# Optimization experiments

Hardware: AMD Instinct MI355X
Metric: run time of the kernel (lower is better)

The kernel has to match this reference:

```python
import jax, jax.numpy as jnp
import numpy as np

N = 40000          # nodes per type (dev, repo)
H, D = 8, 64       # heads, head dim
HID = H * D        # 512 hidden channels
OUT = 256
N_CONVS = 4        # 2 towers (res, link) x 2 layers
EDGE_TYPES = [(0, 1), (1, 0), (0, 0)]  # (src_type, dst_type)
SQRT_D = float(np.sqrt(D))


def _lin(x, w, b):
    return x @ w + b


def _seg_softmax(a, idx, n):
    m = jax.ops.segment_max(a, idx, num_segments=n)
    e = jnp.exp(a - m[idx])
    s = jax.ops.segment_sum(e, idx, num_segments=n)
    return e / (s[idx] + 1e-16)


def _hgt_conv(xs, edges, kw, kb, qw, qb, vw, vb, aw, ab, skip, a_rel, m_rel, p_rel):
    # xs: [x_dev, x_repo] each [N, HID]; edges: list of [2, E]
    k = [_lin(xs[t], kw[t], kb[t]).reshape(-1, H, D) for t in range(2)]
    q = [_lin(xs[t], qw[t], qb[t]).reshape(-1, H, D) for t in range(2)]
    v = [_lin(xs[t], vw[t], vb[t]).reshape(-1, H, D) for t in range(2)]
    out = [jnp.zeros_like(k[0]), jnp.zeros_like(k[1])]
    for r, (st, dt) in enumerate(EDGE_TYPES):
        src, dst = edges[r][0], edges[r][1]
        k_rel = jnp.einsum('nhd,hde->nhe', k[st], a_rel[r])
        v_rel = jnp.einsum('nhd,hde->nhe', v[st], m_rel[r])
        alpha = (q[dt][dst] * k_rel[src]).sum(-1) * p_rel[r] / SQRT_D  # [E, H]
        alpha = _seg_softmax(alpha, dst, N)
        msg = v_rel[src] * alpha[..., None]                            # [E, H, D]
        out[dt] = out[dt] + jax.ops.segment_sum(msg, dst, num_segments=N)
    res = []
    for t in range(2):
        o = _lin(jax.nn.gelu(out[t].reshape(-1, HID), approximate=False), aw[t], ab[t])
        g = jax.nn.sigmoid(skip[t])
        res.append(g * o + (1.0 - g) * xs[t])
    return res


def setup_inputs() -> dict:
    key = jax.random.key(0)
    ks = iter(jax.random.split(key, 48))
    def nrm(shape, scale=1.0):
        return jax.random.normal(next(ks), shape, dtype=jnp.float32) * scale
    E1, E2, E3, EP = 250000, 250000, 150000, 100000
    inp = {}
    inp['x_dev'] = nrm((N, HID))
    inp['x_repo'] = nrm((N, HID))
    inp['ei_dr'] = jax.random.randint(next(ks), (2, E1), 0, N, dtype=jnp.int32)
    inp['ei_rd'] = jax.random.randint(next(ks), (2, E2), 0, N, dtype=jnp.int32)
    inp['ei_dd'] = jax.random.randint(next(ks), (2, E3), 0, N, dtype=jnp.int32)
    inp['pos_edge'] = jax.random.randint(next(ks), (2, EP), 0, N, dtype=jnp.int32)
    inp['neg_edge'] = jax.random.randint(next(ks), (2, EP), 0, N, dtype=jnp.int32)
    s = 1.0 / np.sqrt(HID)
    for nm in ('k', 'q', 'v', 'a'):
        inp[nm + '_w'] = nrm((N_CONVS, 2, HID, HID), s)
        inp[nm + '_b'] = jnp.zeros((N_CONVS, 2, HID), jnp.float32)
    inp['skip'] = jnp.ones((N_CONVS, 2), jnp.float32)
    sd = 1.0 / np.sqrt(D)
    inp['a_rel'] = nrm((N_CONVS, 3, H, D, D), sd)
    inp['m_rel'] = nrm((N_CONVS, 3, H, D, D), sd)
    inp['p_rel'] = jnp.ones((N_CONVS, 3, H), jnp.float32)
    inp['reg_w1'] = nrm((HID, OUT), s); inp['reg_b1'] = jnp.zeros((OUT,), jnp.float32)
    inp['reg_w2'] = nrm((OUT, 1), 1.0 / np.sqrt(OUT)); inp['reg_b2'] = jnp.zeros((1,), jnp.float32)
    inp['src_w'] = nrm((HID, OUT), s); inp['src_b'] = jnp.zeros((OUT,), jnp.float32)
    inp['dst_w'] = nrm((HID, OUT), s); inp['dst_b'] = jnp.zeros((OUT,), jnp.float32)
    inp['fin_w'] = nrm((OUT, 1), 1.0 / np.sqrt(OUT)); inp['fin_b'] = jnp.zeros((1,), jnp.float32)
    return inp


def reference(x_dev, x_repo, ei_dr, ei_rd, ei_dd, pos_edge, neg_edge,
              k_w, k_b, q_w, q_b, v_w, v_b, a_w, a_b, skip,
              a_rel, m_rel, p_rel,
              reg_w1, reg_b1, reg_w2, reg_b2,
              src_w, src_b, dst_w, dst_b, fin_w, fin_b):
    edges = [ei_dr, ei_rd, ei_dd]

    def embed(conv_ids):
        xs = [x_dev, x_repo]
        for c in conv_ids:
            xs = _hgt_conv(xs, edges, k_w[c], k_b[c], q_w[c], q_b[c], v_w[c], v_b[c],
                           a_w[c], a_b[c], skip[c], a_rel[c], m_rel[c], p_rel[c])
            xs = [jax.nn.leaky_relu(x, 0.01) for x in xs]
        return xs

    res = embed([0, 1])   # embedding_res tower
    lnk = embed([2, 3])   # embedding_link tower
    emb_dev = res[0] + lnk[0]
    emb_repo = res[1] + lnk[1]

    fit_dev = _lin(_lin(emb_dev, reg_w1, reg_b1), reg_w2, reg_b2).squeeze(-1)
    fit_repo = _lin(_lin(emb_repo, reg_w1, reg_b1), reg_w2, reg_b2).squeeze(-1)

    def link(zs, zd):
        h = _lin(zs, src_w, src_b) * _lin(zd, dst_w, dst_b)
        return jax.nn.sigmoid(_lin(h, fin_w, fin_b)).squeeze(-1)

    pos = link(emb_dev[pos_edge[0]], emb_repo[pos_edge[1]])
    neg = link(emb_dev[neg_edge[0]], emb_repo[neg_edge[1]])
    score = jnp.concatenate([pos, neg], axis=0)
    return (fit_dev, fit_repo, score)
```

## Files before the change

kernel.cpp:

```cpp
#include <hip/hip_runtime.h>
#include <math.h>

#define NNODES 40000
#define NB ((size_t)20480000)
#define RPS 40004

typedef __attribute__((ext_vector_type(8))) short bf16x8;
typedef __attribute__((ext_vector_type(4))) float f32x4;

__device__ __forceinline__ ushort f2bf(float f) {
  unsigned u = __float_as_uint(f);
  u += 0x7FFFu + ((u >> 16) & 1u);
  return (ushort)(u >> 16);
}
__device__ __forceinline__ float b2f(ushort h) {
  return __uint_as_float((unsigned)h << 16);
}
__device__ __forceinline__ float gelu_f(float x) {
  return 0.5f * x * (1.0f + erff(x * 0.70710678118654752440f));
}

__device__ __forceinline__ void gll16(const ushort* g, ushort* l) {
  __builtin_amdgcn_global_load_lds(
      (const __attribute__((address_space(1))) unsigned int*)(const void*)g,
      (__attribute__((address_space(3))) unsigned int*)(void*)l, 16, 0, 0);
}

template<int EPI>
__global__ __launch_bounds__(256)
void gemm_bf16_kernel(const ushort* __restrict__ Av, const ushort* __restrict__ Bt,
                      const float* __restrict__ bias,
                      ushort* __restrict__ C0, ushort* __restrict__ C1,
                      int M, int PW, int RS,
                      const ushort* __restrict__ xprev, const float* __restrict__ skipv,
                      int nwgx)
{
  const int K = 512;
  __shared__ char smem[32768];
  ushort* Sm = (ushort*)smem;
  float*  Es = (float*)smem;

  const int nwg = (int)gridDim.x;
  const int q8 = nwg >> 3, r8 = nwg & 7;
  const int xcd = (int)blockIdx.x & 7, i8 = (int)blockIdx.x >> 3;
  const int logical = (xcd < r8 ? xcd * (q8 + 1) : r8 * (q8 + 1) + (xcd - r8) * q8) + i8;
  const int bm = (logical / nwgx) * 128;
  const int bnl = (logical % nwgx) * 128;
  const int pan = (bnl >= PW) ? 1 : 0;
  const int bn = bnl - pan * PW;
  ushort* __restrict__ C = pan ? C1 : C0;

  const int tid = threadIdx.x, lane = tid & 63, wave = tid >> 6;
  const int wr = (wave >> 1) * 64, wc = (wave & 1) * 64;
  const int fr = lane & 15, fq = lane >> 4;
  f32x4 acc[4][4] = {};

  const int rdsw = (fq ^ ((fr >> 1) & 3)) * 8;
  const int csrc = ((lane & 3) ^ ((lane >> 3) & 3)) * 8;
  const int r0 = wave * 32 + (lane >> 2);
  int ra0 = bm + r0;      if (ra0 >= M) ra0 = M - 1;
  int ra1 = bm + r0 + 16; if (ra1 >= M) ra1 = M - 1;
  const ushort* ga0 = Av + (size_t)ra0 * K + csrc;
  const ushort* ga1 = Av + (size_t)ra1 * K + csrc;
  const ushort* gb0 = Bt + (size_t)(bnl + r0) * K + csrc;
  const ushort* gb1 = Bt + (size_t)(bnl + r0 + 16) * K + csrc;
  ushort* la0[2] = {Sm + wave * 1024,        Sm + 8192 + wave * 1024};
  ushort* la1[2] = {la0[0] + 512,            la0[1] + 512};
  ushort* lb0[2] = {Sm + 4096 + wave * 1024, Sm + 12288 + wave * 1024};
  ushort* lb1[2] = {lb0[0] + 512,            lb0[1] + 512};

  gll16(ga0, la0[0]); gll16(ga1, la1[0]); gll16(gb0, lb0[0]); gll16(gb1, lb1[0]);
  ga0 += 32; ga1 += 32; gb0 += 32; gb1 += 32;
  gll16(ga0, la0[1]); gll16(ga1, la1[1]); gll16(gb0, lb0[1]); gll16(gb1, lb1[1]);
  ga0 += 32; ga1 += 32; gb0 += 32; gb1 += 32;

  #pragma unroll
  for (int it = 0; it < 16; ++it) {
    const int cur = it & 1;
    if (it < 15) asm volatile("s_waitcnt vmcnt(4)" ::: "memory");
    else         asm volatile("s_waitcnt vmcnt(0)" ::: "memory");
    __builtin_amdgcn_s_barrier();
    const ushort* Ab = Sm + cur * 8192;
    const ushort* Bb = Ab + 4096;
    bf16x8 af[4], bfv[4];
    #pragma unroll
    for (int i = 0; i < 4; ++i) {
      af[i]  = *(const bf16x8*)&Ab[(wr + i * 16 + fr) * 32 + rdsw];
      bfv[i] = *(const bf16x8*)&Bb[(wc + i * 16 + fr) * 32 + rdsw];
    }
    asm volatile("s_waitcnt lgkmcnt(0)" ::: "memory");
    __builtin_amdgcn_s_barrier();
    if (it < 14) {
      gll16(ga0, la0[cur]); gll16(ga1, la1[cur]); gll16(gb0, lb0[cur]); gll16(gb1, lb1[cur]);
      ga0 += 32; ga1 += 32; gb0 += 32; gb1 += 32;
    }
    #pragma unroll
    for (int mi = 0; mi < 4; ++mi)
      #pragma unroll
      for (int ni = 0; ni < 4; ++ni)
        acc[mi][ni] = __builtin_amdgcn_mfma_f32_16x16x32_bf16(af[mi], bfv[ni], acc[mi][ni], 0, 0, 0);
  }
  __syncthreads();

  float gate = 0.f, og = 0.f;
  if (EPI == 2) { gate = 1.f / (1.f + __expf(-skipv[0])); og = 1.f - gate; }
  #pragma unroll
  for (int qr = 0; qr < 4; ++qr) {
    __syncthreads();
    #pragma unroll
    for (int mi = 0; mi < 4; ++mi) {
      if (((wr + mi * 16) >> 5) != qr) continue;
      const int lr = ((wr + mi * 16) & 31) + fq * 4;
      #pragma unroll
      for (int ni = 0; ni < 4; ++ni) {
        const int col = wc + ni * 16 + fr;
        #pragma unroll
        for (int r = 0; r < 4; ++r)
          Es[(lr + r) * 132 + col] = acc[mi][ni][r];
      }
    }
    __syncthreads();
    const int lrow = tid >> 3;
    const int c0 = (tid & 7) * 16;
    const int grow = bm + qr * 32 + lrow;
    if (grow < M) {
      float v[16];
      #pragma unroll
      for (int j = 0; j < 4; ++j)
        *(float4*)&v[j * 4] = *(const float4*)&Es[lrow * 132 + c0 + j * 4];
      if (EPI == 1 || EPI == 2) {
        #pragma unroll
        for (int j = 0; j < 4; ++j) {
          float4 b4 = *(const float4*)(bias + bnl + c0 + j * 4);
          v[j*4] += b4.x; v[j*4+1] += b4.y; v[j*4+2] += b4.z; v[j*4+3] += b4.w;
        }
      }
      size_t base = (size_t)grow * RS + bn + c0;
      if (EPI == 2) {
        uint4 x0 = *(const uint4*)(xprev + base);
        uint4 x1 = *(const uint4*)(xprev + base + 8);
        #pragma unroll
        for (int j = 0; j < 8; ++j) {
          unsigned w = (j < 4) ? ((const unsigned*)&x0)[j] : ((const unsigned*)&x1)[j - 4];
          float a  = gate * v[2*j]   + og * __uint_as_float(w << 16);
          float bq = gate * v[2*j+1] + og * __uint_as_float(w & 0xFFFF0000u);
          v[2*j]   = a  > 0.f ? a  : 0.01f * a;
          v[2*j+1] = bq > 0.f ? bq : 0.01f * bq;
        }
      }
      if (EPI == 4) {
        uint4 x0 = *(const uint4*)(C + base);
        uint4 x1 = *(const uint4*)(C + base + 8);
        #pragma unroll
        for (int j = 0; j < 8; ++j) {
          unsigned w = (j < 4) ? ((const unsigned*)&x0)[j] : ((const unsigned*)&x1)[j - 4];
          v[2*j]   += __uint_as_float(w << 16);
          v[2*j+1] += __uint_as_float(w & 0xFFFF0000u);
        }
      }
      ushort ob[16];
      #pragma unroll
      for (int j = 0; j < 16; ++j) ob[j] = f2bf(v[j]);
      *(uint4*)(C + base)     = *(uint4*)&ob[0];
      *(uint4*)(C + base + 8) = *(uint4*)&ob[8];
    }
  }
}

__global__ __launch_bounds__(256)
void transpose_w_batch(const float* __restrict__ q_w, const float* __restrict__ a_w,
                       const float* __restrict__ src_w, const float* __restrict__ dst_w,
                       ushort* __restrict__ wqT, ushort* __restrict__ waT,
                       ushort* __restrict__ srcwT, ushort* __restrict__ dstwT)
{
  const int z = blockIdx.z;
  const float* W; ushort* Wt; int N;
  if (z < 8)       { W = q_w + (size_t)z * 262144;       Wt = wqT + (size_t)z * 262144;       N = 512; }
  else if (z < 16) { W = a_w + (size_t)(z - 8) * 262144; Wt = waT + (size_t)(z - 8) * 262144; N = 512; }
  else if (z == 16){ W = src_w; Wt = srcwT; N = 256; }
  else             { W = dst_w; Wt = dstwT; N = 256; }
  int bn = blockIdx.x * 32, bk = blockIdx.y * 32;
  if (bn >= N) return;
  __shared__ float t[32][33];
  int x = threadIdx.x & 31, y = threadIdx.x >> 5;
  #pragma unroll
  for (int yy = y; yy < 32; yy += 8) t[yy][x] = W[(size_t)(bk + yy) * N + bn + x];
  __syncthreads();
  #pragma unroll
  for (int yy = y; yy < 32; yy += 8) Wt[(size_t)(bn + yy) * 512 + bk + x] = f2bf(t[x][yy]);
}

__global__ __launch_bounds__(256)
void fold_rel_batch(const float* __restrict__ k_w, const float* __restrict__ k_b,
                    const float* __restrict__ v_w, const float* __restrict__ v_b,
                    const float* __restrict__ a_rel, const float* __restrict__ m_rel,
                    ushort* __restrict__ wkvT, float* __restrict__ bfuse)
{
  const int z = blockIdx.z;
  const int kv = z / 12, i = z % 12;
  const int c = i / 3, r = i % 3;
  const int st_tab[3] = {0, 1, 0};
  const int stp = st_tab[r];
  const float* Win  = (kv ? v_w : k_w) + (size_t)(c * 2 + stp) * 262144;
  const float* bin  = (kv ? v_b : k_b) + (size_t)(c * 2 + stp) * 512;
  const float* Arel = (kv ? m_rel : a_rel) + (size_t)i * 32768;
  const int h = blockIdx.x, kc = blockIdx.y;
  ushort* W2t = wkvT + (size_t)i * 524288 + (size_t)(h >> 2) * 262144
              + (size_t)(kv * 256 + (h & 3) * 64) * 512;
  float*  b2  = bfuse + i * 1024 + (h >> 2) * 512 + kv * 256 + (h & 3) * 64;

  __shared__ float Wl[64][65];
  __shared__ float Al[4096];
  for (int j = threadIdx.x; j < 4096; j += 256) Al[j] = Arel[(size_t)h * 4096 + j];
  {
    const int kk = threadIdx.x >> 2, d0 = (threadIdx.x & 3) * 16;
    const float* src = Win + (size_t)(kc * 64 + kk) * 512 + h * 64 + d0;
    #pragma unroll
    for (int j = 0; j < 4; ++j)
      *(float4*)&Wl[kk][d0 + j * 4] = *(const float4*)(src + j * 4);
  }
  __syncthreads();
  const int wave = threadIdx.x >> 6, lane = threadIdx.x & 63;
  #pragma unroll 4
  for (int rr = 0; rr < 16; ++rr) {
    const int e = wave * 16 + rr;
    float acc = 0.f;
    #pragma unroll
    for (int d = 0; d < 64; ++d) acc = fmaf(Wl[lane][d], Al[d * 64 + e], acc);
    W2t[(size_t)e * 512 + kc * 64 + lane] = f2bf(acc);
  }
  if (kc == 0 && wave == 0) {
    float acc = 0.f;
    #pragma unroll
    for (int d = 0; d < 64; ++d) acc = fmaf(bin[h * 64 + d], Al[d * 64 + lane], acc);
    b2[lane] = acc;
  }
}

__global__ __launch_bounds__(256)
void make_wfit_kernel(const float* __restrict__ w1, const float* __restrict__ b1,
                      const float* __restrict__ w2, const float* __restrict__ b2,
                      float* __restrict__ wfit)
{
  for (int k = threadIdx.x; k < 512; k += 256) {
    float acc = 0.f;
    for (int j = 0; j < 256; ++j) acc = fmaf(w1[(size_t)k * 256 + j], w2[j], acc);
    wfit[k] = acc;
  }
  if (threadIdx.x == 0) {
    float acc = 0.f;
    for (int j = 0; j < 256; ++j) acc = fmaf(b1[j], w2[j], acc);
    wfit[512] = acc + b2[0];
  }
}

__global__ __launch_bounds__(256)
void hist_batch(const int* __restrict__ d0, const int* __restrict__ d1,
                const int* __restrict__ d2, unsigned* __restrict__ cnt3)
{
  const int z = blockIdx.z;
  const int* dst = (z == 0) ? d0 : (z == 1) ? d1 : d2;
  const int E = (z == 2) ? 150000 : 250000;
  unsigned* cnt = cnt3 + (size_t)z * NNODES;
  for (int i = blockIdx.x * 256 + threadIdx.x; i < E; i += gridDim.x * 256)
    atomicAdd(&cnt[dst[i]], 1u);
}

__global__ __launch_bounds__(256)
void scan_batch(const unsigned* __restrict__ cnt3, unsigned* __restrict__ rowptr3,
                unsigned* __restrict__ woff3)
{
  const int z = blockIdx.x;
  const unsigned* cnt = cnt3 + (size_t)z * NNODES;
  unsigned* rowptr = rowptr3 + (size_t)z * RPS;
  unsigned* woff   = woff3 + (size_t)z * NNODES;
  __shared__ unsigned csum[256];
  const int t = threadIdx.x;
  const int lo = t * 160, hi = (lo + 160 < NNODES) ? lo + 160 : NNODES;
  unsigned s = 0;
  for (int i = lo; i < hi; i += 4) {
    uint4 v = *(const uint4*)&cnt[i];
    s += v.x + v.y + v.z + v.w;
  }
  csum[t] = s;
  __syncthreads();
  if (t == 0) {
    unsigned run = 0;
    for (int j = 0; j < 256; ++j) { unsigned v = csum[j]; csum[j] = run; run += v; }
    rowptr[NNODES] = run;
  }
  __syncthreads();
  unsigned run = csum[t];
  for (int i = lo; i < hi; i += 4) {
    uint4 cv = *(const uint4*)&cnt[i];
    uint4 rp;
    rp.x = run; run += cv.x;
    rp.y = run; run += cv.y;
    rp.z = run; run += cv.z;
    rp.w = run; run += cv.w;
    *(uint4*)&rowptr[i] = rp;
    *(uint4*)&woff[i]   = rp;
  }
}

__global__ __launch_bounds__(256)
void fill_batch(const int* __restrict__ e0, const int* __restrict__ e1,
                const int* __restrict__ e2, unsigned* __restrict__ woff3,
                ushort* __restrict__ srcord)
{
  const int z = blockIdx.z;
  const int* e = (z == 0) ? e0 : (z == 1) ? e1 : e2;
  const int E = (z == 2) ? 150000 : 250000;
  const int* src = e;
  const int* dst = e + E;
  unsigned* woff = woff3 + (size_t)z * NNODES;
  ushort* ord = srcord + ((z == 0) ? 0 : (z == 1) ? 250000 : 500000);
  for (int i = blockIdx.x * 256 + threadIdx.x; i < E; i += gridDim.x * 256) {
    unsigned slot = atomicAdd(&woff[dst[i]], 1u);
    ord[slot] = (ushort)src[i];
  }
}

template<int ACCUM, int GELU>
__global__ __launch_bounds__(256)
void fused_edge_kernel(const ushort* __restrict__ q, const ushort* __restrict__ KVh,
                      const unsigned* __restrict__ rowptr, const ushort* __restrict__ srcord,
                      const float* __restrict__ prel, int hs,
                      const ushort* __restrict__ accin, ushort* __restrict__ outp)
{
  int d = (int)((blockIdx.x * 256u + threadIdx.x) >> 6);
  int lane = threadIdx.x & 63;
  if (d >= NNODES) return;
  unsigned start = rowptr[d], end = rowptr[d + 1];
  const int hl = lane >> 4;
  const int off = hl * 64 + (lane & 15) * 4;
  const float pscale = prel[hs * 4 + hl] * 0.125f;
  const size_t obase = (size_t)d * 512 + hs * 256 + off;

  uint2 qv = *(const uint2*)(q + obase);
  float qf0 = __uint_as_float(qv.x << 16),         qf1 = __uint_as_float(qv.x & 0xFFFF0000u);
  float qf2 = __uint_as_float(qv.y << 16),         qf3 = __uint_as_float(qv.y & 0xFFFF0000u);

  float m = -3e38f, ssum = 0.f;
  float a0 = 0.f, a1 = 0.f, a2 = 0.f, a3 = 0.f;
  if (start < end) {
    int sn = (int)srcord[start];
    const ushort* r0 = KVh + (size_t)sn * 512 + off;
    uint2 kv_c = *(const uint2*)r0;
    uint2 vv_c = *(const uint2*)(r0 + 256);
    const unsigned last = end - 1;
    for (unsigned idx = start; idx < end; ++idx) {
      unsigned idxn = (idx < last) ? idx + 1 : last;
      int sn2 = (int)srcord[idxn];
      const ushort* rn = KVh + (size_t)sn2 * 512 + off;
      uint2 kv_n = *(const uint2*)rn;
      uint2 vv_n = *(const uint2*)(rn + 256);
      float dot =      qf0 * __uint_as_float(kv_c.x << 16);
      dot = fmaf(qf1, __uint_as_float(kv_c.x & 0xFFFF0000u), dot);
      dot = fmaf(qf2, __uint_as_float(kv_c.y << 16),         dot);
      dot = fmaf(qf3, __uint_as_float(kv_c.y & 0xFFFF0000u), dot);
      dot += __shfl_xor(dot, 1);
      dot += __shfl_xor(dot, 2);
      dot += __shfl_xor(dot, 4);
      dot += __shfl_xor(dot, 8);
      float a = dot * pscale;
      if (a > m) {
        float r = __expf(m - a);
        ssum *= r; a0 *= r; a1 *= r; a2 *= r; a3 *= r;
        m = a;
      }
      float w = __expf(a - m);
      ssum += w;
      a0 = fmaf(w, __uint_as_float(vv_c.x << 16),         a0);
      a1 = fmaf(w, __uint_as_float(vv_c.x & 0xFFFF0000u), a1);
      a2 = fmaf(w, __uint_as_float(vv_c.y << 16),         a2);
      a3 = fmaf(w, __uint_as_float(vv_c.y & 0xFFFF0000u), a3);
      kv_c = kv_n; vv_c = vv_n;
    }
  }
  float rs = 1.f / (ssum + 1e-16f);
  float o0 = a0 * rs, o1 = a1 * rs, o2 = a2 * rs, o3 = a3 * rs;
  if (ACCUM) {
    uint2 old = *(const uint2*)(accin + obase);
    o0 += __uint_as_float(old.x << 16);  o1 += __uint_as_float(old.x & 0xFFFF0000u);
    o2 += __uint_as_float(old.y << 16);  o3 += __uint_as_float(old.y & 0xFFFF0000u);
  }
  if (GELU) { o0 = gelu_f(o0); o1 = gelu_f(o1); o2 = gelu_f(o2); o3 = gelu_f(o3); }
  uint2 ov;
  ov.x = (unsigned)f2bf(o0) | ((unsigned)f2bf(o1) << 16);
  ov.y = (unsigned)f2bf(o2) | ((unsigned)f2bf(o3) << 16);
  *(uint2*)(outp + obase) = ov;
}

template<int ACCUM, int GELU>
__global__ __launch_bounds__(256)
void fused_edge_full_kernel(const ushort* __restrict__ q, const ushort* __restrict__ KVf,
                            const unsigned* __restrict__ rowptr, const ushort* __restrict__ srcord,
                            const float* __restrict__ prel,
                            const ushort* __restrict__ accin, ushort* __restrict__ outp)
{
  int d = (int)((blockIdx.x * 256u + threadIdx.x) >> 6);
  int lane = threadIdx.x & 63;
  if (d >= NNODES) return;
  unsigned start = rowptr[d], end = rowptr[d + 1];
  const int h = lane >> 3, sub = lane & 7;
  const int koff = (h >> 2) * 512 + (h & 3) * 64 + sub * 8;
  const float pscale = prel[h] * 0.125f;
  const size_t obase = (size_t)d * 512 + h * 64 + sub * 8;

  uint4 qv = *(const uint4*)(q + obase);
  const unsigned* pq = (const unsigned*)&qv;
  float qf[8];
  #pragma unroll
  for (int j = 0; j < 4; ++j) {
    qf[2*j]   = __uint_as_float(pq[j] << 16);
    qf[2*j+1] = __uint_as_float(pq[j] & 0xFFFF0000u);
  }

  float m = -3e38f, ssum = 0.f;
  float av[8] = {};
  if (start < end) {
    int sn = (int)srcord[start];
    const ushort* r0 = KVf + (size_t)sn * 1024 + koff;
    uint4 kv_c = *(const uint4*)r0;
    uint4 vv_c = *(const uint4*)(r0 + 256);
    const unsigned last = end - 1;
    for (unsigned idx = start; idx < end; ++idx) {
      unsigned idxn = (idx < last) ? idx + 1 : last;
      int sn2 = (int)srcord[idxn];
      const ushort* rn = KVf + (size_t)sn2 * 1024 + koff;
      uint4 kv_n = *(const uint4*)rn;
      uint4 vv_n = *(const uint4*)(rn + 256);
      const unsigned* pk = (const unsigned*)&kv_c;
      float dot = 0.f;
      #pragma unroll
      for (int j = 0; j < 4; ++j) {
        dot = fmaf(qf[2*j],   __uint_as_float(pk[j] << 16),         dot);
        dot = fmaf(qf[2*j+1], __uint_as_float(pk[j] & 0xFFFF0000u), dot);
      }
      dot += __shfl_xor(dot, 1);
      dot += __shfl_xor(dot, 2);
      dot += __shfl_xor(dot, 4);
      float a = dot * pscale;
      if (a > m) {
        float r = __expf(m - a);
        ssum *= r;
        #pragma unroll
        for (int j = 0; j < 8; ++j) av[j] *= r;
        m = a;
      }
      float w = __expf(a - m);
      ssum += w;
      const unsigned* pv = (const unsigned*)&vv_c;
      #pragma unroll
      for (int j = 0; j < 4; ++j) {
        av[2*j]   = fmaf(w, __uint_as_float(pv[j] << 16),         av[2*j]);
        av[2*j+1] = fmaf(w, __uint_as_float(pv[j] & 0xFFFF0000u), av[2*j+1]);
      }
      kv_c = kv_n; vv_c = vv_n;
    }
  }
  float rs = 1.f / (ssum + 1e-16f);
  float o[8];
  #pragma unroll
  for (int j = 0; j < 8; ++j) o[j] = av[j] * rs;
  if (ACCUM) {
    uint4 old = *(const uint4*)(accin + obase);
    const unsigned* po = (const unsigned*)&old;
    #pragma unroll
    for (int j = 0; j < 4; ++j) {
      o[2*j]   += __uint_as_float(po[j] << 16);
      o[2*j+1] += __uint_as_float(po[j] & 0xFFFF0000u);
    }
  }
  if (GELU) {
    #pragma unroll
    for (int j = 0; j < 8; ++j) o[j] = gelu_f(o[j]);
  }
  ushort ob[8];
  #pragma unroll
  for (int j = 0; j < 8; ++j) ob[j] = f2bf(o[j]);
  *(uint4*)(outp + obase) = *(uint4*)ob;
}

template<int MODE>
__global__ __launch_bounds__(256)
void fitdot_kernel(const ushort* __restrict__ cur, const float* __restrict__ wfit,
                   float* __restrict__ out, int M)
{
  int row = (int)((blockIdx.x * 256u + threadIdx.x) >> 6);
  int lane = threadIdx.x & 63;
  if (row >= M) return;
  uint4 v = *(const uint4*)(cur + (size_t)row * 512 + lane * 8);
  const unsigned* pv = (const unsigned*)&v;
  float wreg[8];
  *(float4*)wreg       = *(const float4*)(wfit + lane * 8);
  *(float4*)(wreg + 4) = *(const float4*)(wfit + lane * 8 + 4);
  float acc = 0.f;
  #pragma unroll
  for (int j = 0; j < 4; ++j) {
    acc = fmaf(__uint_as_float(pv[j] << 16),         wreg[2 * j],     acc);
    acc = fmaf(__uint_as_float(pv[j] & 0xFFFF0000u), wreg[2 * j + 1], acc);
  }
  #pragma unroll
  for (int off = 1; off < 64; off <<= 1) acc += __shfl_xor(acc, off);
  if (lane == 0) {
    if (MODE == 0) out[row] = acc;
    else           out[row] += acc + wfit[512];
  }
}

__global__ __launch_bounds__(256)
void link_score_kernel(const ushort* __restrict__ se, const ushort* __restrict__ de,
                       const float* __restrict__ sb, const float* __restrict__ db,
                       const int* __restrict__ si, const int* __restrict__ di,
                       int E, const float* __restrict__ fw, const float* __restrict__ fb,
                       float* __restrict__ out)
{
  int wv = (int)((blockIdx.x * 256u + threadIdx.x) >> 6);
  int lane = threadIdx.x & 63;
  if (wv >= E) return;
  int s = si[wv], d = di[wv];
  ushort4 a = *(const ushort4*)(se + (size_t)s * 256 + lane * 4);
  ushort4 b = *(const ushort4*)(de + (size_t)d * 256 + lane * 4);
  float4 s4 = *(const float4*)(sb + lane * 4);
  float4 d4 = *(const float4*)(db + lane * 4);
  float4 w4 = *(const float4*)(fw + lane * 4);
  float acc = (b2f(a.x) + s4.x) * (b2f(b.x) + d4.x) * w4.x
            + (b2f(a.y) + s4.y) * (b2f(b.y) + d4.y) * w4.y
            + (b2f(a.z) + s4.z) * (b2f(b.z) + d4.z) * w4.z
            + (b2f(a.w) + s4.w) * (b2f(b.w) + d4.w) * w4.w;
  #pragma unroll
  for (int off = 1; off < 64; off <<= 1) acc += __shfl_xor(acc, off);
  if (lane == 0) out[wv] = 1.f / (1.f + __expf(-(acc + fb[0])));
}

__global__ __launch_bounds__(256)
void f32_to_bf16_kernel(const float* __restrict__ in, ushort* __restrict__ out, int n4)
{
  for (int i = blockIdx.x * 256 + threadIdx.x; i < n4; i += gridDim.x * 256) {
    float4 v = ((const float4*)in)[i];
    ushort4 o; o.x = f2bf(v.x); o.y = f2bf(v.y); o.z = f2bf(v.z); o.w = f2bf(v.w);
    ((ushort4*)out)[i] = o;
  }
}

__global__ void diag_kernel(float* __restrict__ out, float v)
{
  if (threadIdx.x == 0 && blockIdx.x == 0) out[0] = v;
}

extern "C" void kernel_launch(void* const* d_in, const int* in_sizes, int n_in,
                              void* d_out, int out_size, void* d_ws, size_t ws_size,
                              hipStream_t stream)
{
  const float* x_dev  = (const float*)d_in[0];
  const float* x_repo = (const float*)d_in[1];
  const int* ei[3] = {(const int*)d_in[2], (const int*)d_in[3], (const int*)d_in[4]};
  const int  Ecnt[3] = {250000, 250000, 150000};
  const int* pos_e = (const int*)d_in[5];
  const int* neg_e = (const int*)d_in[6];
  const float* k_w = (const float*)d_in[7];  const float* k_b = (const float*)d_in[8];
  const float* q_w = (const float*)d_in[9];  const float* q_b = (const float*)d_in[10];
  const float* v_w = (const float*)d_in[11]; const float* v_b = (const float*)d_in[12];
  const float* a_w = (const float*)d_in[13]; const float* a_b = (const float*)d_in[14];
  const float* skip  = (const float*)d_in[15];
  const float* a_rel = (const float*)d_in[16];
  const float* m_rel = (const float*)d_in[17];
  const float* p_rel = (const float*)d_in[18];
  const float* reg_w1 = (const float*)d_in[19]; const float* reg_b1 = (const float*)d_in[20];
  const float* reg_w2 = (const float*)d_in[21]; const float* reg_b2 = (const float*)d_in[22];
  const float* src_w  = (const float*)d_in[23]; const float* src_b  = (const float*)d_in[24];
  const float* dst_w  = (const float*)d_in[25]; const float* dst_b  = (const float*)d_in[26];
  const float* fin_w  = (const float*)d_in[27]; const float* fin_b  = (const float*)d_in[28];
  float* out = (float*)d_out;

  const size_t SE = (size_t)NNODES * 256;
  const size_t tail_bytes =
      (size_t)8 * 262144 * 2
    + (size_t)8 * 262144 * 2
    + (size_t)12 * 524288 * 2
    + 131072ull * 2 * 2
    + 12288ull * 4 + 516ull * 4
    + (size_t)3 * RPS * 4
    + 650000ull * 2 + 4
    + (size_t)3 * NNODES * 4 * 2;
  const size_t need_full = (6 * NB + 2 * SE) * 2 + tail_bytes;
  const size_t need_half = (5 * NB + 2 * SE) * 2 + tail_bytes;
  int FULL;
  if      (ws_size >= need_full) FULL = 1;
  else if (ws_size >= need_half) FULL = 0;
  else {
    diag_kernel<<<1, 64, 0, stream>>>(out, 1000.0f + (float)(ws_size / 1000000));
    return;
  }

  ushort* st   = (ushort*)d_ws;
  ushort* cur0 = st;
  ushort* cur1 = st + NB;
  ushort* S1   = st + 2 * NB;
  ushort* S2   = st + 3 * NB;
  ushort* KV   = st + 4 * NB;
  ushort* se   = st + (FULL ? 6 : 5) * NB;
  ushort* de   = se + SE;
  ushort* wqT   = de + SE;
  ushort* waT   = wqT + (size_t)8 * 262144;
  ushort* wkvT  = waT + (size_t)8 * 262144;
  ushort* srcwT = wkvT + (size_t)12 * 524288;
  ushort* dstwT = srcwT + 131072;
  float*  bfuse = (float*)(dstwT + 131072);
  float*  wfit  = bfuse + 12288;
  unsigned* rowptr3 = (unsigned*)(wfit + 516);
  ushort*   srcord  = (ushort*)(rowptr3 + (size_t)3 * RPS);
  unsigned* cnt3    = (unsigned*)(srcord + 650000 + 2);
  unsigned* woff3   = cnt3 + (size_t)3 * NNODES;
  const size_t ord_off[3] = {0, 250000, 500000};

  transpose_w_batch<<<dim3(16, 16, 18), 256, 0, stream>>>(q_w, a_w, src_w, dst_w,
                                                          wqT, waT, srcwT, dstwT);
  fold_rel_batch<<<dim3(8, 8, 24), 256, 0, stream>>>(k_w, k_b, v_w, v_b, a_rel, m_rel,
                                                     wkvT, bfuse);
  make_wfit_kernel<<<1, 256, 0, stream>>>(reg_w1, reg_b1, reg_w2, reg_b2, wfit);
  hipMemsetAsync(cnt3, 0, (size_t)3 * NNODES * 4, stream);
  hist_batch<<<dim3(977, 1, 3), 256, 0, stream>>>(ei[0] + Ecnt[0], ei[1] + Ecnt[1],
                                                  ei[2] + Ecnt[2], cnt3);
  scan_batch<<<3, 256, 0, stream>>>(cnt3, rowptr3, woff3);
  fill_batch<<<dim3(977, 1, 3), 256, 0, stream>>>(ei[0], ei[1], ei[2], woff3, srcord);

  auto gemmQ = [&](const ushort* A, int t, ushort* C) {
    gemm_bf16_kernel<1><<<1252, 256, 0, stream>>>(A, wqT + (size_t)t * 262144,
        q_b + (size_t)t * 512, C, C, NNODES, 512, 512, nullptr, nullptr, 4);
  };
  auto gemmKVh = [&](int i, int hs, const ushort* A) {
    gemm_bf16_kernel<1><<<1252, 256, 0, stream>>>(A,
        wkvT + (size_t)i * 524288 + (size_t)hs * 262144,
        bfuse + (size_t)i * 1024 + hs * 512,
        KV, KV + 256, NNODES, 256, 512, nullptr, nullptr, 4);
  };
  auto gemmKVf = [&](int i, const ushort* A) {
    gemm_bf16_kernel<1><<<2504, 256, 0, stream>>>(A, wkvT + (size_t)i * 524288,
        bfuse + (size_t)i * 1024, KV, KV, NNODES, 1024, 1024, nullptr, nullptr, 8);
  };
  auto gemmA = [&](int t, const ushort* Abuf, ushort* curb) {
    gemm_bf16_kernel<2><<<1252, 256, 0, stream>>>(Abuf, waT + (size_t)t * 262144,
        a_b + (size_t)t * 512, curb, curb, NNODES, 512, 512, curb, skip + t, 4);
  };

  auto run_conv = [&](int c) {
    const int t0 = 2 * c, t1 = 2 * c + 1;
    const int i0 = 3 * c, i1 = 3 * c + 1, i2 = 3 * c + 2;
    gemmQ(cur0, t0, S1);
    if (FULL) {
      gemmKVf(i1, cur1);
      fused_edge_full_kernel<0, 0><<<10000, 256, 0, stream>>>(S1, KV,
          rowptr3 + RPS, srcord + ord_off[1], p_rel + (size_t)i1 * 8, nullptr, S2);
      gemmKVf(i2, cur0);
      fused_edge_full_kernel<1, 1><<<10000, 256, 0, stream>>>(S1, KV,
          rowptr3 + 2 * RPS, srcord + ord_off[2], p_rel + (size_t)i2 * 8, S2, S2);
      gemmKVf(i0, cur0);
      gemmQ(cur1, t1, S1);
      fused_edge_full_kernel<0, 1><<<10000, 256, 0, stream>>>(S1, KV,
          rowptr3, srcord + ord_off[0], p_rel + (size_t)i0 * 8, nullptr, S1);
    } else {
      for (int hs = 0; hs < 2; ++hs) {
        gemmKVh(i1, hs, cur1);
        fused_edge_kernel<0, 0><<<10000, 256, 0, stream>>>(S1, KV,
            rowptr3 + RPS, srcord + ord_off[1], p_rel + (size_t)i1 * 8, hs, nullptr, S2);
      }
      for (int hs = 0; hs < 2; ++hs) {
        gemmKVh(i2, hs, cur0);
        fused_edge_kernel<1, 1><<<10000, 256, 0, stream>>>(S1, KV,
            rowptr3 + 2 * RPS, srcord + ord_off[2], p_rel + (size_t)i2 * 8, hs, S2, S2);
      }
      gemmQ(cur1, t1, S1);
      for (int hs = 0; hs < 2; ++hs) {
        gemmKVh(i0, hs, cur0);
        fused_edge_kernel<0, 1><<<10000, 256, 0, stream>>>(S1, KV,
            rowptr3, srcord + ord_off[0], p_rel + (size_t)i0 * 8, hs, nullptr, S1);
      }
    }
    gemmA(t0, S2, cur0);
    gemmA(t1, S1, cur1);
  };

  f32_to_bf16_kernel<<<2048, 256, 0, stream>>>(x_dev,  cur0, (int)(NB / 4));
  f32_to_bf16_kernel<<<2048, 256, 0, stream>>>(x_repo, cur1, (int)(NB / 4));
  run_conv(0);
  run_conv(1);
  fitdot_kernel<0><<<10000, 256, 0, stream>>>(cur0, wfit, out, NNODES);
  fitdot_kernel<0><<<10000, 256, 0, stream>>>(cur1, wfit, out + NNODES, NNODES);
  gemm_bf16_kernel<3><<<626, 256, 0, stream>>>(cur0, srcwT, nullptr, se, se, NNODES, 256, 256, nullptr, nullptr, 2);
  gemm_bf16_kernel<3><<<626, 256, 0, stream>>>(cur1, dstwT, nullptr, de, de, NNODES, 256, 256, nullptr, nullptr, 2);

  f32_to_bf16_kernel<<<2048, 256, 0, stream>>>(x_dev,  cur0, (int)(NB / 4));
  f32_to_bf16_kernel<<<2048, 256, 0, stream>>>(x_repo, cur1, (int)(NB / 4));
  run_conv(2);
  run_conv(3);
  fitdot_kernel<1><<<10000, 256, 0, stream>>>(cur0, wfit, out, NNODES);
  fitdot_kernel<1><<<10000, 256, 0, stream>>>(cur1, wfit, out + NNODES, NNODES);
  gemm_bf16_kernel<4><<<626, 256, 0, stream>>>(cur0, srcwT, nullptr, se, se, NNODES, 256, 256, nullptr, nullptr, 2);
  gemm_bf16_kernel<4><<<626, 256, 0, stream>>>(cur1, dstwT, nullptr, de, de, NNODES, 256, 256, nullptr, nullptr, 2);

  link_score_kernel<<<25000, 256, 0, stream>>>(se, de, src_b, dst_b, pos_e, pos_e + 100000,
                                               100000, fin_w, fin_b, out + 80000);
  link_score_kernel<<<25000, 256, 0, stream>>>(se, de, src_b, dst_b, neg_e, neg_e + 100000,
                                               100000, fin_w, fin_b, out + 180000);
}
```

Before: 2.669 ms.

## Fuse Q and dev-to-dev KV projections into one wide GEMM, drop half-mode path

Per-conv weights are packed into one arena so the Q projection of dev nodes and the KV projection for the dev-to-dev relation, which share the same input, run as a single 1536-column GEMM writing Q to S1 and KV to the KV buffer. The relation processing order is changed so the dev-to-dev edge kernel runs first, consuming that KV. The GEMM gains a per-panel bias and row stride. The workspace-limited half-width fallback path is removed, which cuts one GEMM launch per conv and reads the input activations once fewer. Workspace too small for the full path now only triggers the diagnostic.

Result: no change. 2.676 ms (+0.3%).

```diff
diff --git a/kernel.cpp b/kernel.cpp
--- a/kernel.cpp
+++ b/kernel.cpp
@@ -4,6 +4,7 @@
 #define NNODES 40000
 #define NB ((size_t)20480000)
 #define RPS 40004
+#define CCH ((size_t)5120 * 512)
 
 typedef __attribute__((ext_vector_type(8))) short bf16x8;
 typedef __attribute__((ext_vector_type(4))) float f32x4;
@@ -29,9 +30,9 @@
 template<int EPI>
 __global__ __launch_bounds__(256)
 void gemm_bf16_kernel(const ushort* __restrict__ Av, const ushort* __restrict__ Bt,
-                      const float* __restrict__ bias,
+                      const float* __restrict__ bias0, const float* __restrict__ bias1,
                       ushort* __restrict__ C0, ushort* __restrict__ C1,
-                      int M, int PW, int RS,
+                      int M, int PW, int RS0, int RS1,
                       const ushort* __restrict__ xprev, const float* __restrict__ skipv,
                       int nwgx)
 {
@@ -48,6 +49,8 @@
   const int bnl = (logical % nwgx) * 128;
   const int pan = (bnl >= PW) ? 1 : 0;
   const int bn = bnl - pan * PW;
+  const int RS = pan ? RS1 : RS0;
+  const float* __restrict__ bp = pan ? bias1 : bias0;
   ushort* __restrict__ C = pan ? C1 : C0;
 
   const int tid = threadIdx.x, lane = tid & 63, wave = tid >> 6;
@@ -131,7 +134,7 @@
       if (EPI == 1 || EPI == 2) {
         #pragma unroll
         for (int j = 0; j < 4; ++j) {
-          float4 b4 = *(const float4*)(bias + bnl + c0 + j * 4);
+          float4 b4 = *(const float4*)(bp + bn + c0 + j * 4);
           v[j*4] += b4.x; v[j*4+1] += b4.y; v[j*4+2] += b4.z; v[j*4+3] += b4.w;
         }
       }
@@ -170,15 +173,23 @@
 __global__ __launch_bounds__(256)
 void transpose_w_batch(const float* __restrict__ q_w, const float* __restrict__ a_w,
                        const float* __restrict__ src_w, const float* __restrict__ dst_w,
-                       ushort* __restrict__ wqT, ushort* __restrict__ waT,
+                       ushort* __restrict__ warena,
                        ushort* __restrict__ srcwT, ushort* __restrict__ dstwT)
 {
   const int z = blockIdx.z;
   const float* W; ushort* Wt; int N;
-  if (z < 8)       { W = q_w + (size_t)z * 262144;       Wt = wqT + (size_t)z * 262144;       N = 512; }
-  else if (z < 16) { W = a_w + (size_t)(z - 8) * 262144; Wt = waT + (size_t)(z - 8) * 262144; N = 512; }
-  else if (z == 16){ W = src_w; Wt = srcwT; N = 256; }
-  else             { W = dst_w; Wt = dstwT; N = 256; }
+  if (z < 8) {
+    int c = z >> 1, t = z & 1;
+    W = q_w + (size_t)z * 262144;
+    Wt = warena + (size_t)c * CCH + (size_t)(t ? 3584 : 0) * 512;
+    N = 512;
+  } else if (z < 16) {
+    int y = z - 8, c = y >> 1, t = y & 1;
+    W = a_w + (size_t)y * 262144;
+    Wt = warena + (size_t)c * CCH + (size_t)(4096 + t * 512) * 512;
+    N = 512;
+  } else if (z == 16) { W = src_w; Wt = srcwT; N = 256; }
+  else                { W = dst_w; Wt = dstwT; N = 256; }
   int bn = blockIdx.x * 32, bk = blockIdx.y * 32;
   if (bn >= N) return;
   __shared__ float t[32][33];
@@ -194,19 +205,20 @@
 void fold_rel_batch(const float* __restrict__ k_w, const float* __restrict__ k_b,
                     const float* __restrict__ v_w, const float* __restrict__ v_b,
                     const float* __restrict__ a_rel, const float* __restrict__ m_rel,
-                    ushort* __restrict__ wkvT, float* __restrict__ bfuse)
+                    ushort* __restrict__ warena, float* __restrict__ bfuse)
 {
   const int z = blockIdx.z;
   const int kv = z / 12, i = z % 12;
   const int c = i / 3, r = i % 3;
   const int st_tab[3] = {0, 1, 0};
   const int stp = st_tab[r];
+  const int roff = (r == 2) ? 512 : (r == 1) ? 1536 : 2560;
   const float* Win  = (kv ? v_w : k_w) + (size_t)(c * 2 + stp) * 262144;
   const float* bin  = (kv ? v_b : k_b) + (size_t)(c * 2 + stp) * 512;
   const float* Arel = (kv ? m_rel : a_rel) + (size_t)i * 32768;
   const int h = blockIdx.x, kc = blockIdx.y;
-  ushort* W2t = wkvT + (size_t)i * 524288 + (size_t)(h >> 2) * 262144
-              + (size_t)(kv * 256 + (h & 3) * 64) * 512;
+  ushort* W2t = warena + (size_t)c * CCH
+              + (size_t)(roff + (h >> 2) * 512 + kv * 256 + (h & 3) * 64) * 512;
   float*  b2  = bfuse + i * 1024 + (h >> 2) * 512 + kv * 256 + (h & 3) * 64;
 
   __shared__ float Wl[64][65];
@@ -319,77 +331,6 @@
     unsigned slot = atomicAdd(&woff[dst[i]], 1u);
     ord[slot] = (ushort)src[i];
   }
-}
-
-template<int ACCUM, int GELU>
-__global__ __launch_bounds__(256)
-void fused_edge_kernel(const ushort* __restrict__ q, const ushort* __restrict__ KVh,
-                      const unsigned* __restrict__ rowptr, const ushort* __restrict__ srcord,
-                      const float* __restrict__ prel, int hs,
-                      const ushort* __restrict__ accin, ushort* __restrict__ outp)
-{
-  int d = (int)((blockIdx.x * 256u + threadIdx.x) >> 6);
-  int lane = threadIdx.x & 63;
-  if (d >= NNODES) return;
-  unsigned start = rowptr[d], end = rowptr[d + 1];
-  const int hl = lane >> 4;
-  const int off = hl * 64 + (lane & 15) * 4;
-  const float pscale = prel[hs * 4 + hl] * 0.125f;
-  const size_t obase = (size_t)d * 512 + hs * 256 + off;
-
-  uint2 qv = *(const uint2*)(q + obase);
-  float qf0 = __uint_as_float(qv.x << 16),         qf1 = __uint_as_float(qv.x & 0xFFFF0000u);
-  float qf2 = __uint_as_float(qv.y << 16),         qf3 = __uint_as_float(qv.y & 0xFFFF0000u);
-
-  float m = -3e38f, ssum = 0.f;
-  float a0 = 0.f, a1 = 0.f, a2 = 0.f, a3 = 0.f;
-  if (start < end) {
-    int sn = (int)srcord[start];
-    const ushort* r0 = KVh + (size_t)sn * 512 + off;
-    uint2 kv_c = *(const uint2*)r0;
-    uint2 vv_c = *(const uint2*)(r0 + 256);
-    const unsigned last = end - 1;
-    for (unsigned idx = start; idx < end; ++idx) {
-      unsigned idxn = (idx < last) ? idx + 1 : last;
-      int sn2 = (int)srcord[idxn];
-      const ushort* rn = KVh + (size_t)sn2 * 512 + off;
-      uint2 kv_n = *(const uint2*)rn;
-      uint2 vv_n = *(const uint2*)(rn + 256);
-      float dot =      qf0 * __uint_as_float(kv_c.x << 16);
-      dot = fmaf(qf1, __uint_as_float(kv_c.x & 0xFFFF0000u), dot);
-      dot = fmaf(qf2, __uint_as_float(kv_c.y << 16),         dot);
-      dot = fmaf(qf3, __uint_as_float(kv_c.y & 0xFFFF0000u), dot);
-      dot += __shfl_xor(dot, 1);
-      dot += __shfl_xor(dot, 2);
-      dot += __shfl_xor(dot, 4);
-      dot += __shfl_xor(dot, 8);
-      float a = dot * pscale;
-      if (a > m) {
-        float r = __expf(m - a);
-        ssum *= r; a0 *= r; a1 *= r; a2 *= r; a3 *= r;
-        m = a;
-      }
-      float w = __expf(a - m);
-      ssum += w;
-      a0 = fmaf(w, __uint_as_float(vv_c.x << 16),         a0);
-      a1 = fmaf(w, __uint_as_float(vv_c.x & 0xFFFF0000u), a1);
-      a2 = fmaf(w, __uint_as_float(vv_c.y << 16),         a2);
-      a3 = fmaf(w, __uint_as_float(vv_c.y & 0xFFFF0000u), a3);
-      kv_c = kv_n; vv_c = vv_n;
-    }
-  }
-  float rs = 1.f / (ssum + 1e-16f);
-  float o0 = a0 * rs, o1 = a1 * rs, o2 = a2 * rs, o3 = a3 * rs;
-  if (ACCUM) {
-    uint2 old = *(const uint2*)(accin + obase);
-    o0 += __uint_as_float(old.x << 16);  o1 += __uint_as_float(old.x & 0xFFFF0000u);
-    o2 += __uint_as_float(old.y << 16);  o3 += __uint_as_float(old.y & 0xFFFF0000u);
-  }
-  if (GELU) { o0 = gelu_f(o0); o1 = gelu_f(o1); o2 = gelu_f(o2); o3 = gelu_f(o3); }
-  uint2 ov;
-  ov.x = (unsigned)f2bf(o0) | ((unsigned)f2bf(o1) << 16);
-  ov.y = (unsigned)f2bf(o2) | ((unsigned)f2bf(o3) << 16);
-  *(uint2*)(outp + obase) = ov;
 }
 
 template<int ACCUM, int GELU>
@@ -576,50 +517,34 @@
   float* out = (float*)d_out;
 
   const size_t SE = (size_t)NNODES * 256;
-  const size_t tail_bytes =
-      (size_t)8 * 262144 * 2
-    + (size_t)8 * 262144 * 2
-    + (size_t)12 * 524288 * 2
-    + 131072ull * 2 * 2
-    + 12288ull * 4 + 516ull * 4
-    + (size_t)3 * RPS * 4
-    + 650000ull * 2 + 4
-    + (size_t)3 * NNODES * 4 * 2;
-  const size_t need_full = (6 * NB + 2 * SE) * 2 + tail_bytes;
-  const size_t need_half = (5 * NB + 2 * SE) * 2 + tail_bytes;
-  int FULL;
-  if      (ws_size >= need_full) FULL = 1;
-  else if (ws_size >= need_half) FULL = 0;
-  else {
-    diag_kernel<<<1, 64, 0, stream>>>(out, 1000.0f + (float)(ws_size / 1000000));
-    return;
-  }
-
   ushort* st   = (ushort*)d_ws;
   ushort* cur0 = st;
   ushort* cur1 = st + NB;
   ushort* S1   = st + 2 * NB;
   ushort* S2   = st + 3 * NB;
   ushort* KV   = st + 4 * NB;
-  ushort* se   = st + (FULL ? 6 : 5) * NB;
+  ushort* se   = st + 6 * NB;
   ushort* de   = se + SE;
-  ushort* wqT   = de + SE;
-  ushort* waT   = wqT + (size_t)8 * 262144;
-  ushort* wkvT  = waT + (size_t)8 * 262144;
-  ushort* srcwT = wkvT + (size_t)12 * 524288;
-  ushort* dstwT = srcwT + 131072;
-  float*  bfuse = (float*)(dstwT + 131072);
-  float*  wfit  = bfuse + 12288;
+  ushort* warena = de + SE;
+  ushort* srcwT  = warena + 4 * CCH;
+  ushort* dstwT  = srcwT + 131072;
+  float*  bfuse  = (float*)(dstwT + 131072);
+  float*  wfit   = bfuse + 12288;
   unsigned* rowptr3 = (unsigned*)(wfit + 516);
   ushort*   srcord  = (ushort*)(rowptr3 + (size_t)3 * RPS);
   unsigned* cnt3    = (unsigned*)(srcord + 650000 + 2);
   unsigned* woff3   = cnt3 + (size_t)3 * NNODES;
+  const size_t need = (size_t)((char*)(woff3 + (size_t)3 * NNODES) - (char*)d_ws);
+  if (ws_size < need) {
+    diag_kernel<<<1, 64, 0, stream>>>(out, 1000.0f + (float)(ws_size / 1000000));
+    return;
+  }
   const size_t ord_off[3] = {0, 250000, 500000};
 
   transpose_w_batch<<<dim3(16, 16, 18), 256, 0, stream>>>(q_w, a_w, src_w, dst_w,
-                                                          wqT, waT, srcwT, dstwT);
+                                                          warena, srcwT, dstwT);
   fold_rel_batch<<<dim3(8, 8, 24), 256, 0, stream>>>(k_w, k_b, v_w, v_b, a_rel, m_rel,
-                                                     wkvT, bfuse);
+                                                     warena, bfuse);
   make_wfit_kernel<<<1, 256, 0, stream>>>(reg_w1, reg_b1, reg_w2, reg_b2, wfit);
   hipMemsetAsync(cnt3, 0, (size_t)3 * NNODES * 4, stream);
   hist_batch<<<dim3(977, 1, 3), 256, 0, stream>>>(ei[0] + Ecnt[0], ei[1] + Ecnt[1],
@@ -627,60 +552,44 @@
   scan_batch<<<3, 256, 0, stream>>>(cnt3, rowptr3, woff3);
   fill_batch<<<dim3(977, 1, 3), 256, 0, stream>>>(ei[0], ei[1], ei[2], woff3, srcord);
 
-  auto gemmQ = [&](const ushort* A, int t, ushort* C) {
-    gemm_bf16_kernel<1><<<1252, 256, 0, stream>>>(A, wqT + (size_t)t * 262144,
-        q_b + (size_t)t * 512, C, C, NNODES, 512, 512, nullptr, nullptr, 4);
+  auto gemmQKV = [&](int c, const ushort* A) {
+    gemm_bf16_kernel<1><<<3756, 256, 0, stream>>>(A, warena + (size_t)c * CCH,
+        q_b + (size_t)(2 * c) * 512, bfuse + (size_t)(3 * c + 2) * 1024,
+        S1, KV, NNODES, 512, 512, 1024, nullptr, nullptr, 12);
   };
-  auto gemmKVh = [&](int i, int hs, const ushort* A) {
-    gemm_bf16_kernel<1><<<1252, 256, 0, stream>>>(A,
-        wkvT + (size_t)i * 524288 + (size_t)hs * 262144,
-        bfuse + (size_t)i * 1024 + hs * 512,
-        KV, KV + 256, NNODES, 256, 512, nullptr, nullptr, 4);
+  auto gemmKV = [&](int c, int roff, int i) {
+    gemm_bf16_kernel<1><<<2504, 256, 0, stream>>>(
+        (roff == 1536) ? cur1 : cur0, warena + (size_t)c * CCH + (size_t)roff * 512,
+        bfuse + (size_t)i * 1024, bfuse + (size_t)i * 1024,
+        KV, KV, NNODES, 1024, 1024, 1024, nullptr, nullptr, 8);
   };
-  auto gemmKVf = [&](int i, const ushort* A) {
-    gemm_bf16_kernel<1><<<2504, 256, 0, stream>>>(A, wkvT + (size_t)i * 524288,
-        bfuse + (size_t)i * 1024, KV, KV, NNODES, 1024, 1024, nullptr, nullptr, 8);
+  auto gemmQ1 = [&](int c) {
+    gemm_bf16_kernel<1><<<1252, 256, 0, stream>>>(cur1,
+        warena + (size_t)c * CCH + (size_t)3584 * 512,
+        q_b + (size_t)(2 * c + 1) * 512, q_b + (size_t)(2 * c + 1) * 512,
+        S1, S1, NNODES, 512, 512, 512, nullptr, nullptr, 4);
   };
-  auto gemmA = [&](int t, const ushort* Abuf, ushort* curb) {
-    gemm_bf16_kernel<2><<<1252, 256, 0, stream>>>(Abuf, waT + (size_t)t * 262144,
-        a_b + (size_t)t * 512, curb, curb, NNODES, 512, 512, curb, skip + t, 4);
+  auto gemmA = [&](int c, int t, const ushort* Abuf, ushort* curb) {
+    gemm_bf16_kernel<2><<<1252, 256, 0, stream>>>(Abuf,
+        warena + (size_t)c * CCH + (size_t)(4096 + t * 512) * 512,
+        a_b + (size_t)(2 * c + t) * 512, a_b + (size_t)(2 * c + t) * 512,
+        curb, curb, NNODES, 512, 512, 512, curb, skip + 2 * c + t, 4);
   };
 
   auto run_conv = [&](int c) {
-    const int t0 = 2 * c, t1 = 2 * c + 1;
     const int i0 = 3 * c, i1 = 3 * c + 1, i2 = 3 * c + 2;
-    gemmQ(cur0, t0, S1);
-    if (FULL) {
-      gemmKVf(i1, cur1);
-      fused_edge_full_kernel<0, 0><<<10000, 256, 0, stream>>>(S1, KV,
-          rowptr3 + RPS, srcord + ord_off[1], p_rel + (size_t)i1 * 8, nullptr, S2);
-      gemmKVf(i2, cur0);
-      fused_edge_full_kernel<1, 1><<<10000, 256, 0, stream>>>(S1, KV,
-          rowptr3 + 2 * RPS, srcord + ord_off[2], p_rel + (size_t)i2 * 8, S2, S2);
-      gemmKVf(i0, cur0);
-      gemmQ(cur1, t1, S1);
-      fused_edge_full_kernel<0, 1><<<10000, 256, 0, stream>>>(S1, KV,
-          rowptr3, srcord + ord_off[0], p_rel + (size_t)i0 * 8, nullptr, S1);
-    } else {
-      for (int hs = 0; hs < 2; ++hs) {
-        gemmKVh(i1, hs, cur1);
-        fused_edge_kernel<0, 0><<<10000, 256, 0, stream>>>(S1, KV,
-            rowptr3 + RPS, srcord + ord_off[1], p_rel + (size_t)i1 * 8, hs, nullptr, S2);
-      }
-      for (int hs = 0; hs < 2; ++hs) {
-        gemmKVh(i2, hs, cur0);
-        fused_edge_kernel<1, 1><<<10000, 256, 0, stream>>>(S1, KV,
-            rowptr3 + 2 * RPS, srcord + ord_off[2], p_rel + (size_t)i2 * 8, hs, S2, S2);
-      }
-      gemmQ(cur1, t1, S1);
-      for (int hs = 0; hs < 2; ++hs) {
-        gemmKVh(i0, hs, cur0);
-        fused_edge_kernel<0, 1><<<10000, 256, 0, stream>>>(S1, KV,
-            rowptr3, srcord + ord_off[0], p_rel + (size_t)i0 * 8, hs, nullptr, S1);
-      }
-    }
-    gemmA(t0, S2, cur0);
-    gemmA(t1, S1, cur1);
+    gemmQKV(c, cur0);
+    fused_edge_full_kernel<0, 0><<<10000, 256, 0, stream>>>(S1, KV,
+        rowptr3 + 2 * RPS, srcord + ord_off[2], p_rel + (size_t)i2 * 8, nullptr, S2);
+    gemmKV(c, 1536, i1);
+    fused_edge_full_kernel<1, 1><<<10000, 256, 0, stream>>>(S1, KV,
+        rowptr3 + RPS, srcord + ord_off[1], p_rel + (size_t)i1 * 8, S2, S2);
+    gemmKV(c, 2560, i0);
+    gemmQ1(c);
+    fused_edge_full_kernel<0, 1><<<10000, 256, 0, stream>>>(S1, KV,
+        rowptr3, srcord + ord_off[0], p_rel + (size_t)i0 * 8, nullptr, S1);
+    gemmA(c, 0, S2, cur0);
+    gemmA(c, 1, S1, cur1);
   };
 
   f32_to_bf16_kernel<<<2048, 256, 0, stream>>>(x_dev,  cur0, (int)(NB / 4));
@@ -689,8 +598,10 @@
   run_conv(1);
   fitdot_kernel<0><<<10000, 256, 0, stream>>>(cur0, wfit, out, NNODES);
   fitdot_kernel<0><<<10000, 256, 0, stream>>>(cur1, wfit, out + NNODES, NNODES);
-  gemm_bf16_kernel<3><<<626, 256, 0, stream>>>(cur0, srcwT, nullptr, se, se, NNODES, 256, 256, nullptr, nullptr, 2);
-  gemm_bf16_kernel<3><<<626, 256, 0, stream>>>(cur1, dstwT, nullptr, de, de, NNODES, 256, 256, nullptr, nullptr, 2);
+  gemm_bf16_kernel<3><<<626, 256, 0, stream>>>(cur0, srcwT, nullptr, nullptr, se, se,
+                                               NNODES, 256, 256, 256, nullptr, nullptr, 2);
+  gemm_bf16_kernel<3><<<626, 256, 0, stream>>>(cur1, dstwT, nullptr, nullptr, de, de,
+                                               NNODES, 256, 256, 256, nullptr, nullptr, 2);
 
   f32_to_bf16_kernel<<<2048, 256, 0, stream>>>(x_dev,  cur0, (int)(NB / 4));
   f32_to_bf16_kernel<<<2048, 256, 0, stream>>>(x_repo, cur1, (int)(NB / 4));
@@ -698,8 +609,10 @@
   run_conv(3);
   fitdot_kernel<1><<<10000, 256, 0, stream>>>(cur0, wfit, out, NNODES);
   fitdot_kernel<1><<<10000, 256, 0, stream>>>(cur1, wfit, out + NNODES, NNODES);
-  gemm_bf16_kernel<4><<<626, 256, 0, stream>>>(cur0, srcwT, nullptr, se, se, NNODES, 256, 256, nullptr, nullptr, 2);
-  gemm_bf16_kernel<4><<<626, 256, 0, stream>>>(cur1, dstwT, nullptr, de, de, NNODES, 256, 256, nullptr, nullptr, 2);
+  gemm_bf16_kernel<4><<<626, 256, 0, stream>>>(cur0, srcwT, nullptr, nullptr, se, se,
+                                               NNODES, 256, 256, 256, nullptr, nullptr, 2);
+  gemm_bf16_kernel<4><<<626, 256, 0, stream>>>(cur1, dstwT, nullptr, nullptr, de, de,
+                                               NNODES, 256, 256, 256, nullptr, nullptr, 2);
 
   link_score_kernel<<<25000, 256, 0, stream>>>(se, de, src_b, dst_b, pos_e, pos_e + 100000,
                                                100000, fin_w, fin_b, out + 80000);
```
